# Optimization experiments

Measured on AMD Instinct MI355X. Metric: run time of the kernel, lower is better.

## Reference

```python
import jax, jax.numpy as jnp
import numpy as np

N_NODES = 50000
N_EDGES = 600000
IN_DIM = 4
HID = 128
N_LAYERS = 6
BN_EPS = 1e-5


def setup_inputs() -> dict:
    key = jax.random.key(0)
    ks = jax.random.split(key, 20)
    x = jax.random.normal(ks[0], (N_NODES, IN_DIM), dtype=jnp.float32)
    edge_index = jax.random.randint(ks[1], (2, N_EDGES), 0, N_NODES, dtype=jnp.int32)
    s = 0.05
    return {
        "x": x,
        "edge_index": edge_index,
        "enc_w": jax.random.normal(ks[2], (IN_DIM, HID), jnp.float32) * s,
        "enc_b": jnp.zeros((HID,), jnp.float32),
        "enc_bn_g": jnp.ones((HID,), jnp.float32),
        "enc_bn_b": jnp.zeros((HID,), jnp.float32),
        "conv_w": jax.random.normal(ks[3], (N_LAYERS, HID, HID), jnp.float32) * s,
        "conv_b": jnp.zeros((N_LAYERS, HID), jnp.float32),
        "bn_g": jnp.ones((N_LAYERS, HID), jnp.float32),
        "bn_b": jnp.zeros((N_LAYERS, HID), jnp.float32),
        "dec_w1": jax.random.normal(ks[4], (HID, HID // 2), jnp.float32) * s,
        "dec_b1": jnp.zeros((HID // 2,), jnp.float32),
        "dec_w2": jax.random.normal(ks[5], (HID // 2, HID // 4), jnp.float32) * s,
        "dec_b2": jnp.zeros((HID // 4,), jnp.float32),
        "dec_w3": jax.random.normal(ks[6], (HID // 4, 1), jnp.float32) * s,
        "dec_b3": jnp.zeros((1,), jnp.float32),
    }


def _batchnorm(h, g, b):
    # training-mode BatchNorm1d over node axis (biased variance, like torch)
    mu = h.mean(axis=0)
    var = jnp.mean(jnp.square(h - mu), axis=0)
    return (h - mu) * jax.lax.rsqrt(var + BN_EPS) * g + b


def _gcn_conv(h, W, b, src, dst, inv_sqrt_deg, n):
    # PyG GCNConv: sym-normalized A+I aggregation, aggregate at dst
    hw = h @ W                                   # [N, HID]
    norm = inv_sqrt_deg[src] * inv_sqrt_deg[dst]  # [E]
    msg = hw[src] * norm[:, None]                # [E, HID] (dominant traffic)
    agg = jax.ops.segment_sum(msg, dst, num_segments=n)
    self_loop = hw * jnp.square(inv_sqrt_deg)[:, None]
    return agg + self_loop + b


def reference(x, edge_index, enc_w, enc_b, enc_bn_g, enc_bn_b,
              conv_w, conv_b, bn_g, bn_b,
              dec_w1, dec_b1, dec_w2, dec_b2, dec_w3, dec_b3):
    n = x.shape[0]
    src, dst = edge_index[0], edge_index[1]
    # degree includes self loop (A + I)
    deg = jax.ops.segment_sum(jnp.ones_like(dst, dtype=x.dtype), dst, num_segments=n) + 1.0
    inv_sqrt_deg = jax.lax.rsqrt(deg)

    # encoder: Linear -> ReLU -> BatchNorm (dropout = identity in eval)
    h = jax.nn.relu(x @ enc_w + enc_b)
    h = _batchnorm(h, enc_bn_g, enc_bn_b)

    for l in range(N_LAYERS):
        h_new = _gcn_conv(h, conv_w[l], conv_b[l], src, dst, inv_sqrt_deg, n)
        h_new = jax.nn.relu(_batchnorm(h_new, bn_g[l], bn_b[l]))
        h = h + h_new  # residual

    # decoder MLP
    d = jax.nn.relu(h @ dec_w1 + dec_b1)
    d = jax.nn.relu(d @ dec_w2 + dec_b2)
    out = d @ dec_w3 + dec_b3
    return out.squeeze(-1)  # [N]
```

## Files before the change

### kernel.cpp

```cpp
#include <hip/hip_runtime.h>

#define BN_EPS 1e-5f

typedef unsigned int uint_t;
typedef unsigned short ushort_t;
typedef short bf16x8 __attribute__((ext_vector_type(8)));
typedef float f32x4 __attribute__((ext_vector_type(4)));

__device__ __forceinline__ float bflo(uint_t v) { return __uint_as_float(v << 16); }
__device__ __forceinline__ float bfhi(uint_t v) { return __uint_as_float(v & 0xffff0000u); }
__device__ __forceinline__ uint_t f2bf(float f) {
    uint_t u = __float_as_uint(f);
    u += 0x7fffu + ((u >> 16) & 1u);
    return u >> 16;
}

__device__ __forceinline__ void acc8(float* a, uint4 g, float w) {
    a[0] = fmaf(bflo(g.x), w, a[0]);
    a[1] = fmaf(bfhi(g.x), w, a[1]);
    a[2] = fmaf(bflo(g.y), w, a[2]);
    a[3] = fmaf(bfhi(g.y), w, a[3]);
    a[4] = fmaf(bflo(g.z), w, a[4]);
    a[5] = fmaf(bfhi(g.z), w, a[5]);
    a[6] = fmaf(bflo(g.w), w, a[6]);
    a[7] = fmaf(bfhi(g.w), w, a[7]);
}


__global__ void count_kernel(const int* __restrict__ ei, int* __restrict__ counts, int E) {
    int e = blockIdx.x * blockDim.x + threadIdx.x;
    if (e < E) atomicAdd(&counts[ei[E + e]], 1);
}

__global__ __launch_bounds__(256) void scan_part(const int* __restrict__ counts,
                                                 int* __restrict__ rowptr, int* __restrict__ bsum,
                                                 float* __restrict__ isd, int n) {
    const int tid = threadIdx.x;
    const int lane = tid & 63, wave = tid >> 6;
    __shared__ int wsum[4];
    int idx0 = blockIdx.x * 2048 + tid * 8;
    int v[8];
    int tsum = 0;
#pragma unroll
    for (int j = 0; j < 8; j++) {
        int i = idx0 + j;
        int c = (i < n) ? counts[i] : 0;
        if (i < n) isd[i] = rsqrtf((float)c + 1.0f);
        v[j] = (i < n) ? (((c + 4) >> 2) << 2) : 0;
        tsum += v[j];
    }
    int incl = tsum;
#pragma unroll
    for (int off = 1; off < 64; off <<= 1) {
        int t = __shfl_up(incl, off, 64);
        if (lane >= off) incl += t;
    }
    if (lane == 63) wsum[wave] = incl;
    __syncthreads();
    int wexcl = 0;
    for (int w2 = 0; w2 < wave; w2++) wexcl += wsum[w2];
    int run = wexcl + (incl - tsum);
#pragma unroll
    for (int j = 0; j < 8; j++) {
        int i = idx0 + j;
        if (i < n) rowptr[i] = run;
        run += v[j];
    }
    if (tid == 255) bsum[blockIdx.x] = run;
}

__global__ void scan_mid(int* __restrict__ bsum, int nb) {
    int lane = threadIdx.x;
    int v = (lane < nb) ? bsum[lane] : 0;
    int incl = v;
#pragma unroll
    for (int off = 1; off < 64; off <<= 1) {
        int t = __shfl_up(incl, off, 64);
        if (lane >= off) incl += t;
    }
    if (lane < nb) bsum[lane] = incl - v;
    if (lane == 63) bsum[nb] = incl;
}

__global__ void scan_add(int* __restrict__ rowptr, const int* __restrict__ bsum, int n, int nb) {
    int i = blockIdx.x * 256 + threadIdx.x;
    if (i < n)
        rowptr[i] += bsum[i >> 11];
    else if (i == n)
        rowptr[n] = bsum[nb];
}

__global__ void scatter_kernel(const int* __restrict__ ei, const int* __restrict__ rowptr,
                               int* __restrict__ cursor, const float* __restrict__ isd,
                               int* __restrict__ srcs, float* __restrict__ coefs, int E) {
    int e = blockIdx.x * blockDim.x + threadIdx.x;
    if (e < E) {
        int s = ei[e], d = ei[E + e];
        int p = atomicAdd(&cursor[d], 1);
        int idx = rowptr[d] + p;
        srcs[idx] = s;
        coefs[idx] = isd[s] * isd[d];
    }
}

__global__ void selfedge_kernel(const int* __restrict__ counts, const int* __restrict__ rowptr,
                                const float* __restrict__ isd, int* __restrict__ srcs,
                                float* __restrict__ coefs, int N) {
    int n = blockIdx.x * blockDim.x + threadIdx.x;
    if (n < N) {
        int pos = rowptr[n] + counts[n];
        int end = rowptr[n + 1];
        float v = isd[n];
        srcs[pos] = n;
        coefs[pos] = v * v;
        for (int p = pos + 1; p < end; p++) {
            srcs[p] = n;
            coefs[p] = 0.f;
        }
    }
}


__global__ void wtrans_kernel(const float* __restrict__ W, ushort_t* __restrict__ Wt) {
    int id = blockIdx.x * 256 + threadIdx.x;
    int l = id >> 14, rem = id & 16383;
    int k = rem >> 7, n = rem & 127;
    Wt[(l << 14) + (n << 7) + k] = f2bf(W[id]);
}


__global__ __launch_bounds__(256) void encoder_kernel(const float* __restrict__ x,
                                                      const float* __restrict__ W,
                                                      const float* __restrict__ b,
                                                      float* __restrict__ h0,
                                                      float* __restrict__ stats, int N) {
    int tid = threadIdx.x;
    int g = blockIdx.x * 256 + tid;
    int total = gridDim.x * 256;
    int c = tid & 127;
    float w0 = W[c], w1 = W[128 + c], w2 = W[256 + c], w3 = W[384 + c], bb = b[c];
    float s = 0.f, q = 0.f;
    int tot = N * 128;
    for (int i = g; i < tot; i += total) {
        int n = i >> 7;
        float4 xv = ((const float4*)x)[n];
        float v = fmaf(xv.x, w0, fmaf(xv.y, w1, fmaf(xv.z, w2, fmaf(xv.w, w3, bb))));
        v = fmaxf(v, 0.f);
        h0[i] = v;
        s += v;
        q += v * v;
    }
    __shared__ float ls[256];
    ls[tid] = s;
    __syncthreads();
    if (tid < 128) atomicAdd(&stats[tid], ls[tid] + ls[tid + 128]);
    __syncthreads();
    ls[tid] = q;
    __syncthreads();
    if (tid < 128) atomicAdd(&stats[128 + tid], ls[tid] + ls[tid + 128]);
}


#define SWZ(byte, row) ((byte) ^ (((row) & 7) << 4))

template <int MODE>
__global__ __launch_bounds__(256) void mfma_gemm(const float* __restrict__ h,
                                                 const ushort_t* __restrict__ aggb,
                                                 const float* __restrict__ stats,
                                                 const float* __restrict__ g,
                                                 const float* __restrict__ beta, float invN,
                                                 const ushort_t* __restrict__ Wt,
                                                 float* __restrict__ hout,
                                                 ushort_t* __restrict__ hwb, int N) {
    __shared__ ushort_t As[64 * 128];
    __shared__ float s_sc[128], s_sh[128];
    const int tid = threadIdx.x;
    const int row0 = blockIdx.x * 64;

    if (tid < 128) {
        float S = stats[tid], Q = stats[tid + 128];
        float mu = S * invN;
        float var = fmaxf(Q * invN - mu * mu, 0.f);
        float rs = rsqrtf(var + BN_EPS);
        float sc = g[tid] * rs;
        s_sc[tid] = sc;
        s_sh[tid] = beta[tid] - mu * sc;
    }
    __syncthreads();

#pragma unroll
    for (int j = 0; j < 4; j++) {
        int idx = (j * 256 + tid) * 8;
        int r = idx >> 7, c = idx & 127;
        int grow = row0 + r;
        float av[8] = {0.f, 0.f, 0.f, 0.f, 0.f, 0.f, 0.f, 0.f};
        if (grow < N) {
            float4 h0 = *(const float4*)&h[(size_t)grow * 128 + c];
            float4 h1 = *(const float4*)&h[(size_t)grow * 128 + c + 4];
            float hv[8] = {h0.x, h0.y, h0.z, h0.w, h1.x, h1.y, h1.z, h1.w};
            if (MODE == 0) {
#pragma unroll
                for (int k = 0; k < 8; k++) av[k] = fmaf(hv[k], s_sc[c + k], s_sh[c + k]);
            } else {
                uint4 ag = *(const uint4*)&aggb[(size_t)grow * 128 + c];
                float ga[8] = {bflo(ag.x), bfhi(ag.x), bflo(ag.y), bfhi(ag.y),
                               bflo(ag.z), bfhi(ag.z), bflo(ag.w), bfhi(ag.w)};
#pragma unroll
                for (int k = 0; k < 8; k++)
                    av[k] = hv[k] + fmaxf(fmaf(ga[k], s_sc[c + k], s_sh[c + k]), 0.f);
            }
            *(float4*)&hout[(size_t)grow * 128 + c] = make_float4(av[0], av[1], av[2], av[3]);
            *(float4*)&hout[(size_t)grow * 128 + c + 4] = make_float4(av[4], av[5], av[6], av[7]);
        }
        uint4 p;
        p.x = f2bf(av[0]) | (f2bf(av[1]) << 16);
        p.y = f2bf(av[2]) | (f2bf(av[3]) << 16);
        p.z = f2bf(av[4]) | (f2bf(av[5]) << 16);
        p.w = f2bf(av[6]) | (f2bf(av[7]) << 16);
        *(uint4*)((char*)As + SWZ(r * 256 + c * 2, r)) = p;
    }
    __syncthreads();

    const int w = tid >> 6, l = tid & 63;
    const int mrow = l & 15, kg = l >> 4;
    const int arow = w * 16 + mrow;
    bf16x8 afr[4];
#pragma unroll
    for (int ks = 0; ks < 4; ks++)
        afr[ks] = *(const bf16x8*)((const char*)As + SWZ(arow * 256 + ks * 64 + kg * 16, arow));

    f32x4 acc[8];
#pragma unroll
    for (int nt = 0; nt < 8; nt++) acc[nt] = (f32x4){0.f, 0.f, 0.f, 0.f};

#pragma unroll
    for (int nt = 0; nt < 8; nt++) {
        const ushort_t* wp = &Wt[(size_t)(nt * 16 + mrow) * 128 + kg * 8];
#pragma unroll
        for (int ks = 0; ks < 4; ks++) {
            bf16x8 bfr = *(const bf16x8*)&wp[ks * 32];
            acc[nt] = __builtin_amdgcn_mfma_f32_16x16x32_bf16(afr[ks], bfr, acc[nt], 0, 0, 0);
        }
    }

#pragma unroll
    for (int nt = 0; nt < 8; nt++) {
#pragma unroll
        for (int r = 0; r < 4; r++) {
            int grow = row0 + w * 16 + kg * 4 + r;
            if (grow < N) hwb[(size_t)grow * 128 + nt * 16 + mrow] = f2bf(acc[nt][r]);
        }
    }
}


template <int K, int NOUT, int MODE, bool RELU>
__global__ __launch_bounds__(256) void fused_gemm(const float* __restrict__ A0,
                                                  const ushort_t* __restrict__ aggb,
                                                  const float* __restrict__ stats,
                                                  const float* __restrict__ g,
                                                  const float* __restrict__ beta, float invN,
                                                  const float* __restrict__ B,
                                                  const float* __restrict__ bias,
                                                  float* __restrict__ Cf, int N) {
    constexpr int TN = NOUT / 16;
    constexpr int LDA = K + 1;
    __shared__ float As[64 * LDA];
    __shared__ float Bs[16 * NOUT];
    __shared__ float s_sc[128], s_sh[128];
    const int tid = threadIdx.x;
    const int row0 = blockIdx.x * 64;

    if (MODE == 1) {
        if (tid < 128) {
            float S = stats[tid], Q = stats[tid + 128];
            float mu = S * invN;
            float var = fmaxf(Q * invN - mu * mu, 0.f);
            float rs = rsqrtf(var + BN_EPS);
            float sc = g[tid] * rs;
            s_sc[tid] = sc;
            s_sh[tid] = beta[tid] - mu * sc;
        }
        __syncthreads();
#pragma unroll
        for (int j = 0; j < 4; j++) {
            int idx = (j * 256 + tid) * 8;
            int r = idx >> 7, c = idx & 127;
            int grow = row0 + r;
            float av[8] = {0.f, 0.f, 0.f, 0.f, 0.f, 0.f, 0.f, 0.f};
            if (grow < N) {
                float4 h0 = *(const float4*)&A0[(size_t)grow * 128 + c];
                float4 h1 = *(const float4*)&A0[(size_t)grow * 128 + c + 4];
                float hv[8] = {h0.x, h0.y, h0.z, h0.w, h1.x, h1.y, h1.z, h1.w};
                uint4 ag = *(const uint4*)&aggb[(size_t)grow * 128 + c];
                float ga[8] = {bflo(ag.x), bfhi(ag.x), bflo(ag.y), bfhi(ag.y),
                               bflo(ag.z), bfhi(ag.z), bflo(ag.w), bfhi(ag.w)};
#pragma unroll
                for (int k = 0; k < 8; k++)
                    av[k] = hv[k] + fmaxf(fmaf(ga[k], s_sc[c + k], s_sh[c + k]), 0.f);
            }
#pragma unroll
            for (int k = 0; k < 8; k++) As[r * LDA + c + k] = av[k];
        }
    } else {
        constexpr int NF4 = 64 * K / 4 / 256;
#pragma unroll
        for (int j = 0; j < NF4; j++) {
            int idx = (j * 256 + tid) * 4;
            int r = idx / K;
            int c = idx % K;
            int grow = row0 + r;
            float4 a = make_float4(0.f, 0.f, 0.f, 0.f);
            if (grow < N) a = *(const float4*)&A0[(size_t)grow * K + c];
            As[r * LDA + c + 0] = a.x;
            As[r * LDA + c + 1] = a.y;
            As[r * LDA + c + 2] = a.z;
            As[r * LDA + c + 3] = a.w;
        }
    }
    __syncthreads();

    float acc[4][TN];
#pragma unroll
    for (int i = 0; i < 4; i++)
#pragma unroll
        for (int j = 0; j < TN; j++) acc[i][j] = 0.f;

    const int tx = tid & 15, ty = tid >> 4;
    for (int k0 = 0; k0 < K; k0 += 16) {
        for (int f = tid; f < 16 * NOUT / 4; f += 256) {
            int r = f / (NOUT / 4), c4 = (f % (NOUT / 4)) * 4;
            *(float4*)&Bs[r * NOUT + c4] = *(const float4*)&B[(size_t)(k0 + r) * NOUT + c4];
        }
        __syncthreads();
#pragma unroll
        for (int kk = 0; kk < 16; ++kk) {
            float a[4], bf[TN];
#pragma unroll
            for (int i = 0; i < 4; i++) a[i] = As[(ty * 4 + i) * LDA + k0 + kk];
#pragma unroll
            for (int j = 0; j < TN; j++) bf[j] = Bs[kk * NOUT + tx * TN + j];
#pragma unroll
            for (int i = 0; i < 4; i++)
#pragma unroll
                for (int j = 0; j < TN; j++) acc[i][j] = fmaf(a[i], bf[j], acc[i][j]);
        }
        __syncthreads();
    }

#pragma unroll
    for (int i = 0; i < 4; i++) {
        int grow = row0 + ty * 4 + i;
        if (grow >= N) continue;
#pragma unroll
        for (int j = 0; j < TN; j++) {
            int c = tx * TN + j;
            float v = acc[i][j];
            if (bias) v += bias[c];
            if (RELU) v = fmaxf(v, 0.f);
            Cf[(size_t)grow * NOUT + c] = v;
        }
    }
}


__global__ __launch_bounds__(256) void agg_kernel(const ushort_t* __restrict__ hwb,
                                                  const int* __restrict__ rowptr,
                                                  const int* __restrict__ srcs,
                                                  const float* __restrict__ coefs,
                                                  ushort_t* __restrict__ aggb,
                                                  float* __restrict__ stats, int N) {
    const int tid = threadIdx.x;
    const int wave = tid >> 6, lane = tid & 63;
    const int cbase = (lane & 15) * 8;
    const int grp = blockIdx.x * 16 + (tid >> 4);
    float s[8], q[8];
#pragma unroll
    for (int j = 0; j < 8; j++) {
        s[j] = 0.f;
        q[j] = 0.f;
    }

    const int n0 = grp * 2;
    if (n0 < N) {
        const int n1 = n0 + 1;
        const bool hasB = n1 < N;
        int ea = rowptr[n0];
        const int eaE = rowptr[n0 + 1];
        int eb = eaE;
        const int ebE = hasB ? rowptr[n1 + 1] : eaE;
        float aA[8] = {0.f, 0.f, 0.f, 0.f, 0.f, 0.f, 0.f, 0.f};
        float aB[8] = {0.f, 0.f, 0.f, 0.f, 0.f, 0.f, 0.f, 0.f};
        while (ea < eaE || eb < ebE) {
            int ca0 = min(ea, eaE - 4), ca1 = min(ea + 4, eaE - 4);
            int cb0 = min(eb, ebE - 4), cb1 = min(eb + 4, ebE - 4);
            int4 svA0 = *(const int4*)&srcs[ca0];
            int4 svA1 = *(const int4*)&srcs[ca1];
            int4 svB0 = *(const int4*)&srcs[cb0];
            int4 svB1 = *(const int4*)&srcs[cb1];
            float4 wvA0 = *(const float4*)&coefs[ca0];
            float4 wvA1 = *(const float4*)&coefs[ca1];
            float4 wvB0 = *(const float4*)&coefs[cb0];
            float4 wvB1 = *(const float4*)&coefs[cb1];
            if (ea >= eaE) wvA0 = make_float4(0.f, 0.f, 0.f, 0.f);
            if (ea + 4 >= eaE && ea < eaE ? false : (ea + 4 >= eaE)) wvA1 = make_float4(0.f, 0.f, 0.f, 0.f);
            if (ea + 4 >= eaE) wvA1 = make_float4(0.f, 0.f, 0.f, 0.f);
            if (eb >= ebE) wvB0 = make_float4(0.f, 0.f, 0.f, 0.f);
            if (eb + 4 >= ebE) wvB1 = make_float4(0.f, 0.f, 0.f, 0.f);
            uint4 gA0 = *(const uint4*)&hwb[(size_t)svA0.x * 128 + cbase];
            uint4 gA1 = *(const uint4*)&hwb[(size_t)svA0.y * 128 + cbase];
            uint4 gA2 = *(const uint4*)&hwb[(size_t)svA0.z * 128 + cbase];
            uint4 gA3 = *(const uint4*)&hwb[(size_t)svA0.w * 128 + cbase];
            uint4 gA4 = *(const uint4*)&hwb[(size_t)svA1.x * 128 + cbase];
            uint4 gA5 = *(const uint4*)&hwb[(size_t)svA1.y * 128 + cbase];
            uint4 gA6 = *(const uint4*)&hwb[(size_t)svA1.z * 128 + cbase];
            uint4 gA7 = *(const uint4*)&hwb[(size_t)svA1.w * 128 + cbase];
            uint4 gB0 = *(const uint4*)&hwb[(size_t)svB0.x * 128 + cbase];
            uint4 gB1 = *(const uint4*)&hwb[(size_t)svB0.y * 128 + cbase];
            uint4 gB2 = *(const uint4*)&hwb[(size_t)svB0.z * 128 + cbase];
            uint4 gB3 = *(const uint4*)&hwb[(size_t)svB0.w * 128 + cbase];
            uint4 gB4 = *(const uint4*)&hwb[(size_t)svB1.x * 128 + cbase];
            uint4 gB5 = *(const uint4*)&hwb[(size_t)svB1.y * 128 + cbase];
            uint4 gB6 = *(const uint4*)&hwb[(size_t)svB1.z * 128 + cbase];
            uint4 gB7 = *(const uint4*)&hwb[(size_t)svB1.w * 128 + cbase];
            acc8(aA, gA0, wvA0.x);
            acc8(aA, gA1, wvA0.y);
            acc8(aA, gA2, wvA0.z);
            acc8(aA, gA3, wvA0.w);
            acc8(aA, gA4, wvA1.x);
            acc8(aA, gA5, wvA1.y);
            acc8(aA, gA6, wvA1.z);
            acc8(aA, gA7, wvA1.w);
            acc8(aB, gB0, wvB0.x);
            acc8(aB, gB1, wvB0.y);
            acc8(aB, gB2, wvB0.z);
            acc8(aB, gB3, wvB0.w);
            acc8(aB, gB4, wvB1.x);
            acc8(aB, gB5, wvB1.y);
            acc8(aB, gB6, wvB1.z);
            acc8(aB, gB7, wvB1.w);
            ea = min(ea + 8, eaE);
            eb = min(eb + 8, ebE);
        }
        uint4 pA;
        pA.x = f2bf(aA[0]) | (f2bf(aA[1]) << 16);
        pA.y = f2bf(aA[2]) | (f2bf(aA[3]) << 16);
        pA.z = f2bf(aA[4]) | (f2bf(aA[5]) << 16);
        pA.w = f2bf(aA[6]) | (f2bf(aA[7]) << 16);
        *(uint4*)&aggb[(size_t)n0 * 128 + cbase] = pA;
#pragma unroll
        for (int j = 0; j < 8; j++) {
            s[j] += aA[j];
            q[j] += aA[j] * aA[j];
        }
        if (hasB) {
            uint4 pB;
            pB.x = f2bf(aB[0]) | (f2bf(aB[1]) << 16);
            pB.y = f2bf(aB[2]) | (f2bf(aB[3]) << 16);
            pB.z = f2bf(aB[4]) | (f2bf(aB[5]) << 16);
            pB.w = f2bf(aB[6]) | (f2bf(aB[7]) << 16);
            *(uint4*)&aggb[(size_t)n1 * 128 + cbase] = pB;
#pragma unroll
            for (int j = 0; j < 8; j++) {
                s[j] += aB[j];
                q[j] += aB[j] * aB[j];
            }
        }
    }

#pragma unroll
    for (int j = 0; j < 8; j++) {
        s[j] += __shfl_xor(s[j], 16, 64);
        s[j] += __shfl_xor(s[j], 32, 64);
        q[j] += __shfl_xor(q[j], 16, 64);
        q[j] += __shfl_xor(q[j], 32, 64);
    }
    __shared__ float ls[4][128];
    if (lane < 16) {
#pragma unroll
        for (int j = 0; j < 8; j++) ls[wave][cbase + j] = s[j];
    }
    __syncthreads();
    if (tid < 128) atomicAdd(&stats[tid], ls[0][tid] + ls[1][tid] + ls[2][tid] + ls[3][tid]);
    __syncthreads();
    if (lane < 16) {
#pragma unroll
        for (int j = 0; j < 8; j++) ls[wave][cbase + j] = q[j];
    }
    __syncthreads();
    if (tid < 128) atomicAdd(&stats[128 + tid], ls[0][tid] + ls[1][tid] + ls[2][tid] + ls[3][tid]);
}


__global__ void dec3_kernel(const float* __restrict__ d2, const float* __restrict__ W3,
                            const float* __restrict__ b3, float* __restrict__ out, int N) {
    __shared__ float tile[64 * 33];
    __shared__ float w3s[32];
    int base = blockIdx.x * 64;
    int tid = threadIdx.x;
    if (tid < 32) w3s[tid] = W3[tid];
    for (int f = tid; f < 2048; f += 256) {
        int r = f >> 5, c = f & 31;
        int n = base + r;
        tile[r * 33 + c] = (n < N) ? d2[(size_t)n * 32 + c] : 0.f;
    }
    __syncthreads();
    if (tid < 64) {
        int n = base + tid;
        if (n < N) {
            float s = b3[0];
#pragma unroll
            for (int k = 0; k < 32; k++) s = fmaf(tile[tid * 33 + k], w3s[k], s);
            out[n] = s;
        }
    }
}


extern "C" void kernel_launch(void* const* d_in, const int* in_sizes, int n_in, void* d_out,
                              int out_size, void* d_ws, size_t ws_size, hipStream_t stream) {
    const float* x = (const float*)d_in[0];
    const int* ei = (const int*)d_in[1];
    const float* enc_w = (const float*)d_in[2];
    const float* enc_b = (const float*)d_in[3];
    const float* enc_bn_g = (const float*)d_in[4];
    const float* enc_bn_b = (const float*)d_in[5];
    const float* conv_w = (const float*)d_in[6];
    const float* bn_g = (const float*)d_in[8];
    const float* bn_b = (const float*)d_in[9];
    const float* dw1 = (const float*)d_in[10];
    const float* db1 = (const float*)d_in[11];
    const float* dw2 = (const float*)d_in[12];
    const float* db2 = (const float*)d_in[13];
    const float* dw3 = (const float*)d_in[14];
    const float* db3 = (const float*)d_in[15];
    float* out = (float*)d_out;

    const int N = in_sizes[0] / 4;
    const int E = in_sizes[1] / 2;
    const size_t N128 = (size_t)N * 128;
    const int EPMAX = E + 4 * N;
    const float invN = 1.0f / N;

    float* h = (float*)d_ws;
    ushort_t* aggb = (ushort_t*)(h + N128);
    ushort_t* hwb = aggb + N128;
    ushort_t* wt = hwb + N128;
    float* stats = (float*)(wt + 6 * 16384);
    float* isd = stats + 7 * 256;
    int* counts = (int*)(isd + N);
    int* rowptr = counts + N;
    int* cursor = rowptr + N + 1;
    int* bsum = cursor + N;
    int* srcs = bsum + 66;
    float* coefs = (float*)(srcs + EPMAX);
    float* d1 = (float*)hwb;
    float* d2 = (float*)aggb;

    (void)hipMemsetAsync(stats, 0, 7 * 256 * sizeof(float), stream);
    (void)hipMemsetAsync(counts, 0, (size_t)N * sizeof(int), stream);
    (void)hipMemsetAsync(cursor, 0, (size_t)N * sizeof(int), stream);

    const int eb = (E + 255) / 256;
    const int nb = (N + 255) / 256;
    const int snb = (N + 2047) / 2048;
    count_kernel<<<eb, 256, 0, stream>>>(ei, counts, E);
    scan_part<<<snb, 256, 0, stream>>>(counts, rowptr, bsum, isd, N);
    scan_mid<<<1, 64, 0, stream>>>(bsum, snb);
    scan_add<<<(N + 256) / 256, 256, 0, stream>>>(rowptr, bsum, N, snb);
    scatter_kernel<<<eb, 256, 0, stream>>>(ei, rowptr, cursor, isd, srcs, coefs, E);
    selfedge_kernel<<<nb, 256, 0, stream>>>(counts, rowptr, isd, srcs, coefs, N);
    wtrans_kernel<<<384, 256, 0, stream>>>(conv_w, wt);

    encoder_kernel<<<1024, 256, 0, stream>>>(x, enc_w, enc_b, h, stats, N);

    const int gblocks = (N + 63) / 64;
    const int ablocks = ((N + 1) / 2 + 15) / 16;

    mfma_gemm<0><<<gblocks, 256, 0, stream>>>(h, nullptr, stats, enc_bn_g, enc_bn_b, invN, wt, h,
                                              hwb, N);
    agg_kernel<<<ablocks, 256, 0, stream>>>(hwb, rowptr, srcs, coefs, aggb, stats + 256, N);

    for (int l = 1; l < 6; l++) {
        mfma_gemm<1><<<gblocks, 256, 0, stream>>>(h, aggb, stats + l * 256, bn_g + (l - 1) * 128,
                                                  bn_b + (l - 1) * 128, invN,
                                                  wt + (size_t)l * 16384, h, hwb, N);
        agg_kernel<<<ablocks, 256, 0, stream>>>(hwb, rowptr, srcs, coefs, aggb,
                                                stats + (l + 1) * 256, N);
    }

    fused_gemm<128, 64, 1, true><<<gblocks, 256, 0, stream>>>(
        h, aggb, stats + 6 * 256, bn_g + 5 * 128, bn_b + 5 * 128, invN, dw1, db1, d1, N);
    fused_gemm<64, 32, 2, true><<<gblocks, 256, 0, stream>>>(d1, nullptr, nullptr, nullptr,
                                                             nullptr, 0.f, dw2, db2, d2, N);
    dec3_kernel<<<gblocks, 256, 0, stream>>>(d2, dw3, db3, out, N);
}
```

Measured before the change: 638.2 us.

## Use atomic work-stealing for aggregation and fold self-edge fill into scan

```diff
diff --git a/kernel.cpp b/kernel.cpp
--- a/kernel.cpp
+++ b/kernel.cpp
@@ -82,12 +82,26 @@
     if (lane == 63) bsum[nb] = incl;
 }
 
-__global__ void scan_add(int* __restrict__ rowptr, const int* __restrict__ bsum, int n, int nb) {
+__global__ void scan_add_self(int* __restrict__ rowptr, const int* __restrict__ bsum,
+                              const int* __restrict__ counts, const float* __restrict__ isd,
+                              int* __restrict__ srcs, float* __restrict__ coefs, int n, int nb) {
     int i = blockIdx.x * 256 + threadIdx.x;
-    if (i < n)
-        rowptr[i] += bsum[i >> 11];
-    else if (i == n)
+    if (i < n) {
+        int rp = rowptr[i] + bsum[i >> 11];
+        rowptr[i] = rp;
+        int c = counts[i];
+        int pos = rp + c;
+        int end = rp + (((c + 4) >> 2) << 2);
+        float v = isd[i];
+        srcs[pos] = i;
+        coefs[pos] = v * v;
+        for (int p = pos + 1; p < end; p++) {
+            srcs[p] = i;
+            coefs[p] = 0.f;
+        }
+    } else if (i == n) {
         rowptr[n] = bsum[nb];
+    }
 }
 
 __global__ void scatter_kernel(const int* __restrict__ ei, const int* __restrict__ rowptr,
@@ -100,23 +114,6 @@
         int idx = rowptr[d] + p;
         srcs[idx] = s;
         coefs[idx] = isd[s] * isd[d];
-    }
-}
-
-__global__ void selfedge_kernel(const int* __restrict__ counts, const int* __restrict__ rowptr,
-                                const float* __restrict__ isd, int* __restrict__ srcs,
-                                float* __restrict__ coefs, int N) {
-    int n = blockIdx.x * blockDim.x + threadIdx.x;
-    if (n < N) {
-        int pos = rowptr[n] + counts[n];
-        int end = rowptr[n + 1];
-        float v = isd[n];
-        srcs[pos] = n;
-        coefs[pos] = v * v;
-        for (int p = pos + 1; p < end; p++) {
-            srcs[p] = n;
-            coefs[p] = 0.f;
-        }
     }
 }
 
@@ -369,11 +366,11 @@
                                                   const int* __restrict__ srcs,
                                                   const float* __restrict__ coefs,
                                                   ushort_t* __restrict__ aggb,
-                                                  float* __restrict__ stats, int N) {
+                                                  float* __restrict__ stats,
+                                                  int* __restrict__ ticket, int npairs, int N) {
     const int tid = threadIdx.x;
     const int wave = tid >> 6, lane = tid & 63;
     const int cbase = (lane & 15) * 8;
-    const int grp = blockIdx.x * 16 + (tid >> 4);
     float s[8], q[8];
 #pragma unroll
     for (int j = 0; j < 8; j++) {
@@ -381,8 +378,12 @@
         q[j] = 0.f;
     }
 
-    const int n0 = grp * 2;
-    if (n0 < N) {
+    for (;;) {
+        int p;
+        if ((lane & 15) == 0) p = atomicAdd(ticket, 1);
+        p = __shfl(p, lane & 48, 64);
+        if (p >= npairs) break;
+        const int n0 = p * 2;
         const int n1 = n0 + 1;
         const bool hasB = n1 < N;
         int ea = rowptr[n0];
@@ -403,7 +404,6 @@
             float4 wvB0 = *(const float4*)&coefs[cb0];
             float4 wvB1 = *(const float4*)&coefs[cb1];
             if (ea >= eaE) wvA0 = make_float4(0.f, 0.f, 0.f, 0.f);
-            if (ea + 4 >= eaE && ea < eaE ? false : (ea + 4 >= eaE)) wvA1 = make_float4(0.f, 0.f, 0.f, 0.f);
             if (ea + 4 >= eaE) wvA1 = make_float4(0.f, 0.f, 0.f, 0.f);
             if (eb >= ebE) wvB0 = make_float4(0.f, 0.f, 0.f, 0.f);
             if (eb + 4 >= ebE) wvB1 = make_float4(0.f, 0.f, 0.f, 0.f);
@@ -541,13 +541,15 @@
     const size_t N128 = (size_t)N * 128;
     const int EPMAX = E + 4 * N;
     const float invN = 1.0f / N;
+    const int npairs = (N + 1) / 2;
 
     float* h = (float*)d_ws;
     ushort_t* aggb = (ushort_t*)(h + N128);
     ushort_t* hwb = aggb + N128;
     ushort_t* wt = hwb + N128;
     float* stats = (float*)(wt + 6 * 16384);
-    float* isd = stats + 7 * 256;
+    int* tickets = (int*)(stats + 7 * 256);
+    float* isd = (float*)(tickets + 8);
     int* counts = (int*)(isd + N);
     int* rowptr = counts + N;
     int* cursor = rowptr + N + 1;
@@ -557,36 +559,35 @@
     float* d1 = (float*)hwb;
     float* d2 = (float*)aggb;
 
-    (void)hipMemsetAsync(stats, 0, 7 * 256 * sizeof(float), stream);
+    (void)hipMemsetAsync(stats, 0, (7 * 256) * sizeof(float) + 8 * sizeof(int), stream);
     (void)hipMemsetAsync(counts, 0, (size_t)N * sizeof(int), stream);
     (void)hipMemsetAsync(cursor, 0, (size_t)N * sizeof(int), stream);
 
     const int eb = (E + 255) / 256;
-    const int nb = (N + 255) / 256;
     const int snb = (N + 2047) / 2048;
     count_kernel<<<eb, 256, 0, stream>>>(ei, counts, E);
     scan_part<<<snb, 256, 0, stream>>>(counts, rowptr, bsum, isd, N);
     scan_mid<<<1, 64, 0, stream>>>(bsum, snb);
-    scan_add<<<(N + 256) / 256, 256, 0, stream>>>(rowptr, bsum, N, snb);
+    scan_add_self<<<(N + 256) / 256, 256, 0, stream>>>(rowptr, bsum, counts, isd, srcs, coefs, N,
+                                                       snb);
     scatter_kernel<<<eb, 256, 0, stream>>>(ei, rowptr, cursor, isd, srcs, coefs, E);
-    selfedge_kernel<<<nb, 256, 0, stream>>>(counts, rowptr, isd, srcs, coefs, N);
     wtrans_kernel<<<384, 256, 0, stream>>>(conv_w, wt);
 
     encoder_kernel<<<1024, 256, 0, stream>>>(x, enc_w, enc_b, h, stats, N);
 
     const int gblocks = (N + 63) / 64;
-    const int ablocks = ((N + 1) / 2 + 15) / 16;
 
     mfma_gemm<0><<<gblocks, 256, 0, stream>>>(h, nullptr, stats, enc_bn_g, enc_bn_b, invN, wt, h,
                                               hwb, N);
-    agg_kernel<<<ablocks, 256, 0, stream>>>(hwb, rowptr, srcs, coefs, aggb, stats + 256, N);
+    agg_kernel<<<1024, 256, 0, stream>>>(hwb, rowptr, srcs, coefs, aggb, stats + 256, &tickets[0],
+                                         npairs, N);
 
     for (int l = 1; l < 6; l++) {
         mfma_gemm<1><<<gblocks, 256, 0, stream>>>(h, aggb, stats + l * 256, bn_g + (l - 1) * 128,
                                                   bn_b + (l - 1) * 128, invN,
                                                   wt + (size_t)l * 16384, h, hwb, N);
-        agg_kernel<<<ablocks, 256, 0, stream>>>(hwb, rowptr, srcs, coefs, aggb,
-                                                stats + (l + 1) * 256, N);
+        agg_kernel<<<1024, 256, 0, stream>>>(hwb, rowptr, srcs, coefs, aggb,
+                                             stats + (l + 1) * 256, &tickets[l], npairs, N);
     }
 
     fused_gemm<128, 64, 1, true><<<gblocks, 256, 0, stream>>>(
```

Measured after the change: 1.098 ms. 1.72x slower.
